# Performance work log

Measured on AMD Instinct MI355X. Metric: run time of the kernel, lower is better.

The kernel has to match this reference:

```python
import jax, jax.numpy as jnp
import numpy as np
import math

B, N, C, H = 64, 197, 768, 12
D = C // H
MLP = 4 * C
TOKEN_KEEP = 0.7
ATTN_KEEP = 0.7
LN_EPS = 1e-5
ATTN_EPS = 1e-6
NUM_KEEP = math.ceil((N - 1) * TOKEN_KEEP)           # 138 kept patch tokens
NUM_KEEP_ATTN = math.ceil(NUM_KEEP * ATTN_KEEP)      # kept attention entries per row


def setup_inputs() -> dict:
    key = jax.random.key(0)
    ks = jax.random.split(key, 12)
    s = 0.02
    return {
        "x": jax.random.normal(ks[0], (B, N, C), jnp.float32),
        "attn_mask": jnp.ones((B, N, N), jnp.float32),
        "norm1_g": jnp.ones((C,), jnp.float32),
        "norm1_b": jnp.zeros((C,), jnp.float32),
        "qkv_w": jax.random.normal(ks[1], (C, 3 * C), jnp.float32) * s,
        "qkv_b": jnp.zeros((3 * C,), jnp.float32),
        "proj_w": jax.random.normal(ks[2], (C, C), jnp.float32) * s,
        "proj_b": jnp.zeros((C,), jnp.float32),
        "norm2_g": jnp.ones((C,), jnp.float32),
        "norm2_b": jnp.zeros((C,), jnp.float32),
        "fc1_w": jax.random.normal(ks[3], (C, MLP), jnp.float32) * s,
        "fc1_b": jnp.zeros((MLP,), jnp.float32),
        "fc2_w": jax.random.normal(ks[4], (MLP, C), jnp.float32) * s,
        "fc2_b": jnp.zeros((C,), jnp.float32),
    }


def _layernorm(x, g, b):
    mu = jnp.mean(x, axis=-1, keepdims=True)
    var = jnp.mean(jnp.square(x - mu), axis=-1, keepdims=True)
    return (x - mu) * jax.lax.rsqrt(var + LN_EPS) * g + b


def reference(x, attn_mask, norm1_g, norm1_b, qkv_w, qkv_b, proj_w, proj_b,
              norm2_g, norm2_b, fc1_w, fc1_b, fc2_w, fc2_b):
    scale = D ** (-0.5)
    h = _layernorm(x, norm1_g, norm1_b)
    qkv = (h @ qkv_w + qkv_b).reshape(B, N, 3, H, D).transpose(2, 0, 3, 1, 4)
    q, k, v = qkv[0], qkv[1], qkv[2]                       # [B,H,N,D]

    scores = jnp.einsum("bhnd,bhmd->bhnm", q, k) * scale   # [B,H,N,N]
    scores = scores - jnp.max(scores, axis=-1, keepdims=True)
    attn = jnp.exp(scores.astype(jnp.float32)) * attn_mask[:, None].astype(jnp.float32)
    attn = (attn + ATTN_EPS / N) / (jnp.sum(attn, axis=-1, keepdims=True) + ATTN_EPS)

    x_att = jnp.einsum("bhnm,bhmd->bhnd", attn, v).transpose(0, 2, 1, 3).reshape(B, N, C)
    x_att = x_att @ proj_w + proj_b

    cls_attn = jnp.sum(attn[:, :, 0, 1:], axis=1) / H      # [B, N-1]
    patch_attn = jnp.sum(attn[:, :, 1:, 1:], axis=1) / H   # [B, N-1, N-1]

    x = x + x_att

    # token pruning: keep top NUM_KEEP patches by cls attention
    _, token_idx = jax.lax.top_k(cls_attn, NUM_KEEP)       # [B, NUM_KEEP]
    x_patches = jnp.take_along_axis(x[:, 1:], token_idx[:, :, None], axis=1)
    x = jnp.concatenate([x[:, 0:1], x_patches], axis=1)    # [B, NUM_KEEP+1, C]

    # attention pruning: binary mask from topk of pruned patch attention
    pp = jnp.take_along_axis(patch_attn, token_idx[:, :, None], axis=1)
    pp = jnp.take_along_axis(pp, token_idx[:, None, :], axis=2)   # [B, rN, rN]
    top_val, _ = jax.lax.top_k(pp, NUM_KEEP_ATTN)
    mask_p = (pp >= top_val[:, :, -1:]).astype(jnp.float32)
    new_mask = jnp.ones((B, NUM_KEEP + 1, NUM_KEEP + 1), jnp.float32)
    new_mask = new_mask.at[:, 1:, 1:].set(mask_p)

    h2 = _layernorm(x, norm2_g, norm2_b)
    mlp = jax.nn.gelu(h2 @ fc1_w + fc1_b, approximate=False) @ fc2_w + fc2_b
    x = x + mlp
    return x, token_idx, new_mask, cls_attn
```

## Files before the change

kernel.cpp:

```cpp
#include <hip/hip_runtime.h>
#include <hip/hip_bf16.h>
#include <math.h>

#define BB 64
#define NN 197
#define CC 768
#define HH 12
#define MLPD 3072
#define NKEEP 138
#define NKEEPA 97
#define NPATCH 196
#define NOUT_TOK 139
#define STILE 25

typedef __attribute__((ext_vector_type(8))) short bf16x8;
typedef __attribute__((ext_vector_type(4))) float f32x4;

static __device__ inline ushort f2bf(float f) {
    __hip_bfloat16 h = __float2bfloat16(f);
    return *(ushort*)&h;
}
static __device__ inline float bf2f(ushort u) {
    __hip_bfloat16 h;
    *(ushort*)&h = u;
    return __bfloat162float(h);
}

__device__ inline double exp64(double x) {
    const double L2E    = 1.4426950408889634074;
    const double LN2_HI = 6.93147180369123816490e-01;
    const double LN2_LO = 1.90821492927058770002e-10;
    double nf = rint(x * L2E);
    double r  = fma(-nf, LN2_HI, x);
    r = fma(-nf, LN2_LO, r);
    double p = 1.0 / 3628800.0;
    p = fma(p, r, 1.0 / 362880.0);
    p = fma(p, r, 1.0 / 40320.0);
    p = fma(p, r, 1.0 / 5040.0);
    p = fma(p, r, 1.0 / 720.0);
    p = fma(p, r, 1.0 / 120.0);
    p = fma(p, r, 1.0 / 24.0);
    p = fma(p, r, 1.0 / 6.0);
    p = fma(p, r, 0.5);
    p = fma(p, r, 1.0);
    p = fma(p, r, 1.0);
    long long bits = ((long long)(1023 + (int)nf)) << 52;
    return p * __longlong_as_double(bits);
}

__device__ inline double wave_max64(double v) {
#pragma unroll
    for (int o = 32; o; o >>= 1) v = fmax(v, __shfl_xor(v, o));
    return v;
}
__device__ inline double wave_sum64(double v) {
#pragma unroll
    for (int o = 32; o; o >>= 1) v += __shfl_xor(v, o);
    return v;
}

__global__ __launch_bounds__(256) void ln_kernel(const float* __restrict__ in,
                                                 const float* __restrict__ g,
                                                 const float* __restrict__ b,
                                                 float* __restrict__ out32,
                                                 ushort* __restrict__ out16) {
    const int row = blockIdx.x;
    const int t = threadIdx.x;
    const float* xr = in + (size_t)row * CC;
    __shared__ double red[256];
    __shared__ double mu_s, inv_s;

    double s = 0.0;
    for (int c = t; c < CC; c += 256) s += (double)xr[c];
    red[t] = s;
    __syncthreads();
    for (int st = 128; st > 0; st >>= 1) {
        if (t < st) red[t] += red[t + st];
        __syncthreads();
    }
    if (t == 0) mu_s = red[0] * (1.0 / CC);
    __syncthreads();
    const double mu = mu_s;

    double vs = 0.0;
    for (int c = t; c < CC; c += 256) {
        double d = (double)xr[c] - mu;
        vs += d * d;
    }
    red[t] = vs;
    __syncthreads();
    for (int st = 128; st > 0; st >>= 1) {
        if (t < st) red[t] += red[t + st];
        __syncthreads();
    }
    if (t == 0) inv_s = 1.0 / sqrt(red[0] * (1.0 / CC) + 1e-5);
    __syncthreads();
    const double inv = inv_s;

    for (int c = t; c < CC; c += 256) {
        float v = (float)(((double)xr[c] - mu) * inv * (double)g[c] + (double)b[c]);
        if (out32) out32[(size_t)row * CC + c] = v;
        if (out16) out16[(size_t)row * CC + c] = f2bf(v);
    }
}

__global__ __launch_bounds__(256) void gemm_qk_kernel(const float* __restrict__ A,
                                                      const float* __restrict__ Bw,
                                                      const float* __restrict__ bias,
                                                      float* __restrict__ C,
                                                      int K, int ldb, int ldc) {
    __shared__ float As[16][132];
    __shared__ float Bs[16][68];
    const int tid = threadIdx.x;
    const int tx = tid & 15;
    const int ty = tid >> 4;
    const int m0 = blockIdx.y * 128;
    const int n0 = blockIdx.x * 64;

    const int a_k = tid & 15, a_g = tid >> 4;
    const int b_n = tid & 63, b_kg = tid >> 6;

    float acc[8][4];
    double dacc[8][4];
#pragma unroll
    for (int i = 0; i < 8; i++)
#pragma unroll
        for (int j = 0; j < 4; j++) { acc[i][j] = 0.f; dacc[i][j] = 0.0; }

    float a_reg[8], b_reg[4];
#pragma unroll
    for (int i = 0; i < 8; i++)
        a_reg[i] = A[(size_t)(m0 + a_g * 8 + i) * 768 + a_k];
#pragma unroll
    for (int i = 0; i < 4; i++)
        b_reg[i] = Bw[(size_t)(b_kg * 4 + i) * ldb + n0 + b_n];

    for (int k0 = 0; k0 < K; k0 += 16) {
        __syncthreads();
        *(float4*)&As[a_k][a_g * 8]     = make_float4(a_reg[0], a_reg[1], a_reg[2], a_reg[3]);
        *(float4*)&As[a_k][a_g * 8 + 4] = make_float4(a_reg[4], a_reg[5], a_reg[6], a_reg[7]);
#pragma unroll
        for (int i = 0; i < 4; i++) Bs[b_kg * 4 + i][b_n] = b_reg[i];
        __syncthreads();
        if (k0 + 16 < K) {
#pragma unroll
            for (int i = 0; i < 8; i++)
                a_reg[i] = A[(size_t)(m0 + a_g * 8 + i) * 768 + k0 + 16 + a_k];
#pragma unroll
            for (int i = 0; i < 4; i++)
                b_reg[i] = Bw[(size_t)(k0 + 16 + b_kg * 4 + i) * ldb + n0 + b_n];
        }
#pragma unroll
        for (int k = 0; k < 16; k++) {
            float4 a0 = *(const float4*)&As[k][ty * 8];
            float4 a1 = *(const float4*)&As[k][ty * 8 + 4];
            float4 bv = *(const float4*)&Bs[k][tx * 4];
            float a_[8] = {a0.x, a0.y, a0.z, a0.w, a1.x, a1.y, a1.z, a1.w};
            float b_[4] = {bv.x, bv.y, bv.z, bv.w};
#pragma unroll
            for (int i = 0; i < 8; i++)
#pragma unroll
                for (int j = 0; j < 4; j++)
                    acc[i][j] = fmaf(a_[i], b_[j], acc[i][j]);
        }
#pragma unroll
        for (int i = 0; i < 8; i++)
#pragma unroll
            for (int j = 0; j < 4; j++) { dacc[i][j] += (double)acc[i][j]; acc[i][j] = 0.f; }
    }

#pragma unroll
    for (int i = 0; i < 8; i++) {
        const int row = m0 + ty * 8 + i;
#pragma unroll
        for (int j = 0; j < 4; j++) {
            const int col = n0 + tx * 4 + j;
            C[(size_t)row * ldc + col] = (float)(dacc[i][j] + (double)bias[col]);
        }
    }
}

template <int MODE, bool OUT_BF16>
__global__ __launch_bounds__(512) void mfma_gemm(const ushort* __restrict__ A,
                                                 const ushort* __restrict__ Bt,
                                                 const float* __restrict__ bias,
                                                 const float* __restrict__ res,
                                                 void* __restrict__ Cout,
                                                 int M, int K, int Nc) {
    __shared__ ushort As[128][40];
    __shared__ ushort Bs[128][40];
    const int tid = threadIdx.x;
    const int w = tid >> 6, lane = tid & 63;
    const int m0 = blockIdx.y * 128, n0 = blockIdx.x * 128;
    const int wr = w >> 2, wc = w & 3;
    const int sr = tid >> 2, sk = (tid & 3) * 8;
    const int lr = lane & 15, lq = lane >> 4;
    const int kq = lq * 8;

    f32x4 acc[4][2];
#pragma unroll
    for (int i = 0; i < 4; i++)
#pragma unroll
        for (int j = 0; j < 2; j++) acc[i][j] = (f32x4){0.f, 0.f, 0.f, 0.f};

    bf16x8 a_pre = *(const bf16x8*)&A[(size_t)(m0 + sr) * K + sk];
    bf16x8 b_pre = *(const bf16x8*)&Bt[(size_t)(n0 + sr) * K + sk];

    for (int k0 = 0; k0 < K; k0 += 32) {
        __syncthreads();
        *(bf16x8*)&As[sr][sk] = a_pre;
        *(bf16x8*)&Bs[sr][sk] = b_pre;
        __syncthreads();
        if (k0 + 32 < K) {
            a_pre = *(const bf16x8*)&A[(size_t)(m0 + sr) * K + k0 + 32 + sk];
            b_pre = *(const bf16x8*)&Bt[(size_t)(n0 + sr) * K + k0 + 32 + sk];
        }

        bf16x8 af[4], bfr[2];
#pragma unroll
        for (int i = 0; i < 4; i++) af[i] = *(const bf16x8*)&As[wr * 64 + i * 16 + lr][kq];
#pragma unroll
        for (int j = 0; j < 2; j++) bfr[j] = *(const bf16x8*)&Bs[wc * 32 + j * 16 + lr][kq];
#pragma unroll
        for (int i = 0; i < 4; i++)
#pragma unroll
            for (int j = 0; j < 2; j++)
                acc[i][j] = __builtin_amdgcn_mfma_f32_16x16x32_bf16(af[i], bfr[j], acc[i][j], 0, 0, 0);
    }

#pragma unroll
    for (int i = 0; i < 4; i++)
#pragma unroll
        for (int j = 0; j < 2; j++)
#pragma unroll
            for (int r = 0; r < 4; r++) {
                const int row = m0 + wr * 64 + i * 16 + lq * 4 + r;
                if (row >= M) continue;
                const int col = n0 + wc * 32 + j * 16 + lr;
                float v = acc[i][j][r] + bias[col];
                if (MODE == 1) v += res[(size_t)row * Nc + col];
                if (MODE == 2) v = 0.5f * v * (1.0f + erff(v * 0.70710678118654752f));
                if (OUT_BF16) ((ushort*)Cout)[(size_t)row * Nc + col] = f2bf(v);
                else ((float*)Cout)[(size_t)row * Nc + col] = v;
            }
}

__global__ __launch_bounds__(256) void transw_kernel(const float* __restrict__ W, int ldw,
                                                     ushort* __restrict__ Wt, int K) {
    __shared__ float tile[32][33];
    const int n0 = blockIdx.x * 32, k0 = blockIdx.y * 32;
    const int tx = threadIdx.x & 31, ty = threadIdx.x >> 5;
#pragma unroll
    for (int r = 0; r < 32; r += 8)
        tile[ty + r][tx] = W[(size_t)(k0 + ty + r) * ldw + n0 + tx];
    __syncthreads();
#pragma unroll
    for (int r = 0; r < 32; r += 8)
        Wt[(size_t)(n0 + ty + r) * K + k0 + tx] = f2bf(tile[tx][ty + r]);
}

#define KSTR 72
#define PSTR 232
__global__ __launch_bounds__(512) void attn_kernel(const float* __restrict__ qk,
                                                   const ushort* __restrict__ vbf,
                                                   const float* __restrict__ amask,
                                                   ushort* __restrict__ xatt_bf,
                                                   double* __restrict__ cls64,
                                                   double* __restrict__ patch64) {
    const int tile = blockIdx.x;
    const int b = blockIdx.y;
    const int row0 = tile * STILE;
    const int nrows = min(STILE, NN - row0);
    const int t = threadIdx.x;
    const int w = t >> 6, lane = t & 63;

    __shared__ __align__(16) char pool[63136];
    float*  Kf = (float*)pool;
    float*  Qf = (float*)(pool + 56736);
    ushort* Vt = (ushort*)pool;
    ushort* Pb = (ushort*)(pool + 32768);

    int mcol[4], mc[4];
    bool mok[4];
#pragma unroll
    for (int c = 0; c < 4; c++) {
        mcol[c] = lane + 64 * c;
        mok[c] = mcol[c] < NN;
        mc[c] = mok[c] ? mcol[c] : 0;
    }
    int rloc[4];
    bool rok[4];
#pragma unroll
    for (int rr = 0; rr < 4; rr++) {
        rloc[rr] = w + 8 * rr;
        rok[rr] = rloc[rr] < nrows;
    }

    float mv[4][4];
#pragma unroll
    for (int rr = 0; rr < 4; rr++)
#pragma unroll
        for (int c = 0; c < 4; c++)
            mv[rr][c] = (rok[rr] && mok[c])
                ? amask[((size_t)(b * NN + row0 + rloc[rr])) * NN + mcol[c]] : 0.f;

    const int rt = w >> 2, ct = w & 3;
    const int lr = lane & 15, lq = lane >> 4;

    double hacc[4][4] = {};

    for (int h = 0; h < HH; ++h) {
        __syncthreads();
        for (int idx = t; idx < NN * 16; idx += 512) {
            int m = idx >> 4, dq = (idx & 15) * 4;
            *(float4*)&Kf[m * KSTR + dq] =
                *(const float4*)&qk[((size_t)(b * NN + m)) * 1536 + 768 + h * 64 + dq];
        }
        for (int idx = t; idx < nrows * 64; idx += 512) {
            int r = idx >> 6, d = idx & 63;
            Qf[r * 64 + d] = qk[((size_t)(b * NN + row0 + r)) * 1536 + h * 64 + d];
        }
        __syncthreads();

        double s[4][4] = {};
        {
            float facc[4][4] = {};
            for (int d0 = 0; d0 < 64; d0 += 4) {
                float4 qv[4];
#pragma unroll
                for (int rr = 0; rr < 4; rr++)
                    qv[rr] = rok[rr] ? *(const float4*)&Qf[rloc[rr] * 64 + d0]
                                     : make_float4(0.f, 0.f, 0.f, 0.f);
#pragma unroll
                for (int c = 0; c < 4; c++) {
                    float4 kv = *(const float4*)&Kf[mc[c] * KSTR + d0];
#pragma unroll
                    for (int rr = 0; rr < 4; rr++) {
                        facc[rr][c] = fmaf(qv[rr].x, kv.x,
                                      fmaf(qv[rr].y, kv.y,
                                      fmaf(qv[rr].z, kv.z,
                                      fmaf(qv[rr].w, kv.w, facc[rr][c]))));
                    }
                }
                if ((d0 & 4) == 4) {
#pragma unroll
                    for (int rr = 0; rr < 4; rr++)
#pragma unroll
                        for (int c = 0; c < 4; c++) {
                            s[rr][c] += (double)facc[rr][c];
                            facc[rr][c] = 0.f;
                        }
                }
            }
        }
        __syncthreads();

#pragma unroll
        for (int rr = 0; rr < 4; rr++) {
            if (!rok[rr]) continue;
            double sc[4];
#pragma unroll
            for (int c = 0; c < 4; c++)
                sc[c] = mok[c] ? s[rr][c] * 0.125 : -1.0e300;
            double mx = fmax(fmax(sc[0], sc[1]), fmax(sc[2], sc[3]));
            mx = wave_max64(mx);
            double e[4];
#pragma unroll
            for (int c = 0; c < 4; c++)
                e[c] = mok[c] ? exp64(sc[c] - mx) * (double)mv[rr][c] : 0.0;
            double S = wave_sum64(e[0] + e[1] + e[2] + e[3]);
            double inv = 1.0 / (S + 1e-6);
            const double epsn = 1e-6 / 197.0;
#pragma unroll
            for (int c = 0; c < 4; c++) {
                if (!mok[c]) continue;
                double pr = (e[c] + epsn) * inv;
                Pb[rloc[rr] * PSTR + mcol[c]] = f2bf((float)pr);
                hacc[rr][c] += pr;
            }
        }
        for (int idx = t; idx < 32 * 27; idx += 512) {
            int r = idx / 27, m = 197 + idx % 27;
            Pb[r * PSTR + m] = 0;
        }
        for (int idx = t; idx < (32 - nrows) * 197; idx += 512) {
            int r = nrows + idx / 197, m = idx % 197;
            Pb[r * PSTR + m] = 0;
        }
        for (int idx = t; idx < NN * 32; idx += 512) {
            int m = idx >> 5, d2 = (idx & 31) * 2;
            ushort2 v2 = *(const ushort2*)&vbf[((size_t)(b * NN + m)) * CC + h * 64 + d2];
            Vt[d2 * PSTR + m] = v2.x;
            Vt[(d2 + 1) * PSTR + m] = v2.y;
        }
        for (int idx = t; idx < 64 * 27; idx += 512) {
            int d = idx / 27, m = 197 + idx % 27;
            Vt[d * PSTR + m] = 0;
        }
        __syncthreads();

        f32x4 acc = (f32x4){0.f, 0.f, 0.f, 0.f};
#pragma unroll
        for (int k0 = 0; k0 < 224; k0 += 32) {
            bf16x8 pa = *(const bf16x8*)&Pb[(rt * 16 + lr) * PSTR + k0 + lq * 8];
            bf16x8 vb = *(const bf16x8*)&Vt[(ct * 16 + lr) * PSTR + k0 + lq * 8];
            acc = __builtin_amdgcn_mfma_f32_16x16x32_bf16(pa, vb, acc, 0, 0, 0);
        }
#pragma unroll
        for (int rg = 0; rg < 4; rg++) {
            const int row = rt * 16 + lq * 4 + rg;
            if (row < nrows)
                xatt_bf[((size_t)(b * NN + row0 + row)) * CC + h * 64 + ct * 16 + lr] =
                    f2bf(acc[rg]);
        }
    }

#pragma unroll
    for (int rr = 0; rr < 4; rr++) {
        if (!rok[rr]) continue;
        const int grow = row0 + rloc[rr];
#pragma unroll
        for (int c = 0; c < 4; c++) {
            if (!mok[c] || mcol[c] < 1) continue;
            double v = hacc[rr][c] * (1.0 / 12.0);
            if (grow == 0)
                cls64[(size_t)b * NPATCH + mcol[c] - 1] = v;
            else
                patch64[((size_t)b * NPATCH + grow - 1) * NPATCH + (mcol[c] - 1)] = v;
        }
    }
}

__global__ __launch_bounds__(256) void topk_kernel(const double* __restrict__ cls,
                                                   int* __restrict__ tok,
                                                   float* __restrict__ tok_f,
                                                   float* __restrict__ out_cls) {
    const int b = blockIdx.x;
    const int t = threadIdx.x;
    __shared__ double v[NPATCH];
    if (t < NPATCH) {
        v[t] = cls[(size_t)b * NPATCH + t];
        out_cls[(size_t)b * NPATCH + t] = (float)v[t];
    }
    __syncthreads();
    if (t < NPATCH) {
        const double mvv = v[t];
        int cnt = 0;
        for (int i = 0; i < NPATCH; ++i) {
            double vi = v[i];
            cnt += (vi > mvv) || (vi == mvv && i < t);
        }
        if (cnt < NKEEP) {
            tok[b * NKEEP + cnt] = t;
            tok_f[b * NKEEP + cnt] = (float)t;
        }
    }
}

__global__ __launch_bounds__(256) void gather_kernel(const float* __restrict__ x,
                                                     const ushort* __restrict__ xatt_bf,
                                                     const int* __restrict__ tok,
                                                     float* __restrict__ xp,
                                                     ushort* __restrict__ xattp) {
    const int i = blockIdx.x;
    const int b = blockIdx.y;
    const int t = threadIdx.x;
    const int src = (i == 0) ? 0 : (1 + tok[b * NKEEP + i - 1]);
    const float* sx = x + ((size_t)b * NN + src) * CC;
    float* dx = xp + ((size_t)b * NOUT_TOK + i) * CC;
    for (int c = t; c < CC; c += 256) dx[c] = sx[c];
    const ushort* sa = xatt_bf + ((size_t)b * NN + src) * CC;
    ushort* da = xattp + ((size_t)b * NOUT_TOK + i) * CC;
    for (int c = t; c < CC; c += 256) da[c] = sa[c];
}

__global__ __launch_bounds__(256) void mask_kernel(const double* __restrict__ patch,
                                                   const int* __restrict__ tok,
                                                   float* __restrict__ omask) {
    const int i = blockIdx.x;
    const int b = blockIdx.y;
    const int t = threadIdx.x;
    float* orow = omask + ((size_t)b * NOUT_TOK + i) * NOUT_TOK;
    if (i == 0) {
        if (t < NOUT_TOK) orow[t] = 1.f;
        return;
    }
    __shared__ int tj[NKEEP];
    __shared__ double pr[NKEEP];
    if (t < NKEEP) tj[t] = tok[b * NKEEP + t];
    __syncthreads();
    const int ti = tj[i - 1];
    if (t < NKEEP) pr[t] = patch[((size_t)b * NPATCH + ti) * NPATCH + tj[t]];
    __syncthreads();
    if (t == 255) orow[0] = 1.f;
    if (t < NKEEP) {
        const double val = pr[t];
        int cnt = 0;
        for (int l = 0; l < NKEEP; ++l) cnt += (pr[l] > val);
        orow[1 + t] = (cnt < NKEEPA) ? 1.f : 0.f;
    }
}

extern "C" void kernel_launch(void* const* d_in, const int* in_sizes, int n_in,
                              void* d_out, int out_size, void* d_ws, size_t ws_size,
                              hipStream_t stream) {
    const float* x      = (const float*)d_in[0];
    const float* amask  = (const float*)d_in[1];
    const float* n1g    = (const float*)d_in[2];
    const float* n1b    = (const float*)d_in[3];
    const float* qkv_w  = (const float*)d_in[4];
    const float* qkv_b  = (const float*)d_in[5];
    const float* proj_w = (const float*)d_in[6];
    const float* proj_b = (const float*)d_in[7];
    const float* n2g    = (const float*)d_in[8];
    const float* n2b    = (const float*)d_in[9];
    const float* fc1_w  = (const float*)d_in[10];
    const float* fc1_b  = (const float*)d_in[11];
    const float* fc2_w  = (const float*)d_in[12];
    const float* fc2_b  = (const float*)d_in[13];

    float* ws = (float*)d_ws;
    const size_t A_OFF = 0;
    const size_t C_OFF = 9682944;
    const size_t B_OFF = 14524416;
    const size_t D_OFF = 33890304;
    const size_t E_OFF = 38731776;
    const size_t F_OFF = 43573248;
    const size_t G_OFF = 48490496;
    const size_t H_OFF = 48515584;
    const size_t I_OFF = 48524416;

    float*  h        = ws + A_OFF;
    ushort* mlp_bf   = (ushort*)(ws + A_OFF);
    ushort* h_bf     = (ushort*)(ws + C_OFF);
    float*  qk       = ws + B_OFF;
    float*  xp       = ws + B_OFF;
    ushort* xattp_bf = (ushort*)(ws + B_OFF + 6832128);
    ushort* h2_bf    = (ushort*)(ws + B_OFF + 10248192);
    ushort* v_bf     = (ushort*)(ws + D_OFF);
    ushort* xatt_bf  = (ushort*)(ws + E_OFF);
    double* patch64  = (double*)(ws + F_OFF);
    ushort* fc1_t    = (ushort*)(ws + F_OFF);
    ushort* fc2_t    = (ushort*)(ws + F_OFF + 1179648);
    double* cls64    = (double*)(ws + G_OFF);
    int*    tok      = (int*)(ws + H_OFF);
    ushort* wv_t     = (ushort*)(ws + I_OFF);
    ushort* proj_t   = (ushort*)(ws + I_OFF + 294912);

    float* out_x   = (float*)d_out;
    float* out_idx = out_x + 6832128;
    float* out_msk = out_idx + 8832;
    float* out_cls = out_msk + 1236544;

    const int ROWS1 = BB * NN;
    const int ROWS2 = BB * NOUT_TOK;

    ln_kernel<<<ROWS1, 256, 0, stream>>>(x, n1g, n1b, h, h_bf);
    transw_kernel<<<dim3(24, 24), 256, 0, stream>>>(qkv_w + 1536, 2304, wv_t, 768);
    transw_kernel<<<dim3(24, 24), 256, 0, stream>>>(proj_w, 768, proj_t, 768);
    gemm_qk_kernel<<<dim3(1536 / 64, 12672 / 128), 256, 0, stream>>>(
        h, qkv_w, qkv_b, qk, 768, 2304, 1536);
    mfma_gemm<0, true><<<dim3(768 / 128, 12672 / 128), 512, 0, stream>>>(
        h_bf, wv_t, qkv_b + 1536, nullptr, v_bf, ROWS1, 768, 768);
    attn_kernel<<<dim3(8, BB), 512, 0, stream>>>(qk, v_bf, amask, xatt_bf, cls64, patch64);
    topk_kernel<<<BB, 256, 0, stream>>>(cls64, tok, out_idx, out_cls);
    gather_kernel<<<dim3(NOUT_TOK, BB), 256, 0, stream>>>(x, xatt_bf, tok, xp, xattp_bf);
    mfma_gemm<1, false><<<dim3(768 / 128, 8960 / 128), 512, 0, stream>>>(
        xattp_bf, proj_t, proj_b, xp, xp, ROWS2, 768, 768);
    mask_kernel<<<dim3(NOUT_TOK, BB), 256, 0, stream>>>(patch64, tok, out_msk);
    transw_kernel<<<dim3(96, 24), 256, 0, stream>>>(fc1_w, 3072, fc1_t, 768);
    transw_kernel<<<dim3(24, 96), 256, 0, stream>>>(fc2_w, 768, fc2_t, 3072);
    ln_kernel<<<ROWS2, 256, 0, stream>>>(xp, n2g, n2b, nullptr, h2_bf);
    mfma_gemm<2, true><<<dim3(3072 / 128, 8960 / 128), 512, 0, stream>>>(
        h2_bf, fc1_t, fc1_b, nullptr, mlp_bf, ROWS2, 768, 3072);
    mfma_gemm<1, false><<<dim3(768 / 128, 8960 / 128), 512, 0, stream>>>(
        mlp_bf, fc2_t, fc2_b, xp, out_x, ROWS2, 3072, 768);
}
```

Measured before the change: 1.283 ms.

## Enlarge attention row tile, shuffle-based layernorm, vectorize gather

The attention kernel now processes 32 query rows per block instead of 25, so the grid drops from 8 to 7 tiles per batch and K/V staging is shared across more rows. The K padding stride shrinks and the shared pool is resized to fit. LayerNorm replaces its shared-memory tree reduction with wave shuffles and keeps the three row values in registers. The gather kernel uses float4/uint2 vector copies. Together these cut redundant K/V loads, barriers and memory instructions, but a larger row tile may raise register pressure, and the changed K stride may alter LDS bank conflicts.

```diff
diff --git a/kernel.cpp b/kernel.cpp
--- a/kernel.cpp
+++ b/kernel.cpp
@@ -11,7 +11,7 @@
 #define NKEEPA 97
 #define NPATCH 196
 #define NOUT_TOK 139
-#define STILE 25
+#define STILE 32
 
 typedef __attribute__((ext_vector_type(8))) short bf16x8;
 typedef __attribute__((ext_vector_type(4))) float f32x4;
@@ -66,41 +66,32 @@
                                                  ushort* __restrict__ out16) {
     const int row = blockIdx.x;
     const int t = threadIdx.x;
+    const int lane = t & 63, w = t >> 6;
     const float* xr = in + (size_t)row * CC;
-    __shared__ double red[256];
-    __shared__ double mu_s, inv_s;
-
-    double s = 0.0;
-    for (int c = t; c < CC; c += 256) s += (double)xr[c];
-    red[t] = s;
-    __syncthreads();
-    for (int st = 128; st > 0; st >>= 1) {
-        if (t < st) red[t] += red[t + st];
-        __syncthreads();
-    }
-    if (t == 0) mu_s = red[0] * (1.0 / CC);
-    __syncthreads();
-    const double mu = mu_s;
-
-    double vs = 0.0;
-    for (int c = t; c < CC; c += 256) {
-        double d = (double)xr[c] - mu;
-        vs += d * d;
-    }
-    red[t] = vs;
-    __syncthreads();
-    for (int st = 128; st > 0; st >>= 1) {
-        if (t < st) red[t] += red[t + st];
-        __syncthreads();
-    }
-    if (t == 0) inv_s = 1.0 / sqrt(red[0] * (1.0 / CC) + 1e-5);
-    __syncthreads();
-    const double inv = inv_s;
-
-    for (int c = t; c < CC; c += 256) {
-        float v = (float)(((double)xr[c] - mu) * inv * (double)g[c] + (double)b[c]);
-        if (out32) out32[(size_t)row * CC + c] = v;
-        if (out16) out16[(size_t)row * CC + c] = f2bf(v);
+    __shared__ double wred[4];
+
+    const float v0 = xr[t], v1 = xr[t + 256], v2 = xr[t + 512];
+    double s = (double)v0 + (double)v1 + (double)v2;
+    s = wave_sum64(s);
+    if (lane == 0) wred[w] = s;
+    __syncthreads();
+    const double mu = (wred[0] + wred[1] + wred[2] + wred[3]) * (1.0 / CC);
+
+    const double d0 = (double)v0 - mu, d1 = (double)v1 - mu, d2 = (double)v2 - mu;
+    double vs = d0 * d0 + d1 * d1 + d2 * d2;
+    vs = wave_sum64(vs);
+    __syncthreads();
+    if (lane == 0) wred[w] = vs;
+    __syncthreads();
+    const double inv = 1.0 / sqrt((wred[0] + wred[1] + wred[2] + wred[3]) * (1.0 / CC) + 1e-5);
+
+    const int cs[3] = {t, t + 256, t + 512};
+    const double dv[3] = {d0, d1, d2};
+#pragma unroll
+    for (int i = 0; i < 3; i++) {
+        float v = (float)(dv[i] * inv * (double)g[cs[i]] + (double)b[cs[i]]);
+        if (out32) out32[(size_t)row * CC + cs[i]] = v;
+        if (out16) out16[(size_t)row * CC + cs[i]] = f2bf(v);
     }
 }
 
@@ -259,7 +250,7 @@
         Wt[(size_t)(n0 + ty + r) * K + k0 + tx] = f2bf(tile[tx][ty + r]);
 }
 
-#define KSTR 72
+#define KSTR 68
 #define PSTR 232
 __global__ __launch_bounds__(512) void attn_kernel(const float* __restrict__ qk,
                                                    const ushort* __restrict__ vbf,
@@ -274,9 +265,9 @@
     const int t = threadIdx.x;
     const int w = t >> 6, lane = t & 63;
 
-    __shared__ __align__(16) char pool[63136];
+    __shared__ __align__(16) char pool[61776];
     float*  Kf = (float*)pool;
-    float*  Qf = (float*)(pool + 56736);
+    float*  Qf = (float*)(pool + 53584);
     ushort* Vt = (ushort*)pool;
     ushort* Pb = (ushort*)(pool + 32768);
 
@@ -383,7 +374,7 @@
             int r = idx / 27, m = 197 + idx % 27;
             Pb[r * PSTR + m] = 0;
         }
-        for (int idx = t; idx < (32 - nrows) * 197; idx += 512) {
+        for (int idx = t; idx < (STILE - nrows) * 197; idx += 512) {
             int r = nrows + idx / 197, m = idx % 197;
             Pb[r * PSTR + m] = 0;
         }
@@ -468,10 +459,12 @@
     const int src = (i == 0) ? 0 : (1 + tok[b * NKEEP + i - 1]);
     const float* sx = x + ((size_t)b * NN + src) * CC;
     float* dx = xp + ((size_t)b * NOUT_TOK + i) * CC;
-    for (int c = t; c < CC; c += 256) dx[c] = sx[c];
     const ushort* sa = xatt_bf + ((size_t)b * NN + src) * CC;
     ushort* da = xattp + ((size_t)b * NOUT_TOK + i) * CC;
-    for (int c = t; c < CC; c += 256) da[c] = sa[c];
+    if (t < 192) {
+        ((float4*)dx)[t] = ((const float4*)sx)[t];
+        ((uint2*)da)[t] = ((const uint2*)sa)[t];
+    }
 }
 
 __global__ __launch_bounds__(256) void mask_kernel(const double* __restrict__ patch,
@@ -562,7 +555,7 @@
         h, qkv_w, qkv_b, qk, 768, 2304, 1536);
     mfma_gemm<0, true><<<dim3(768 / 128, 12672 / 128), 512, 0, stream>>>(
         h_bf, wv_t, qkv_b + 1536, nullptr, v_bf, ROWS1, 768, 768);
-    attn_kernel<<<dim3(8, BB), 512, 0, stream>>>(qk, v_bf, amask, xatt_bf, cls64, patch64);
+    attn_kernel<<<dim3(7, BB), 512, 0, stream>>>(qk, v_bf, amask, xatt_bf, cls64, patch64);
     topk_kernel<<<BB, 256, 0, stream>>>(cls64, tok, out_idx, out_cls);
     gather_kernel<<<dim3(NOUT_TOK, BB), 256, 0, stream>>>(x, xatt_bf, tok, xp, xattp_bf);
     mfma_gemm<1, false><<<dim3(768 / 128, 8960 / 128), 512, 0, stream>>>(
```

After: 1.288 ms. No clear change (+0.5%).
